# Kernel tuning notes

Hardware: AMD Instinct MI355X
Metric: run time of the kernel (lower is better)

## Reference

```python
import jax, jax.numpy as jnp
import numpy as np

N = 6144      # nodes
NFEAT = 512
NHID = 256
NHEADS = 4
DHEAD = NHID // NHEADS  # 64
NEMBED = 128
NEG_INF = -9e15
LRELU_ALPHA = 0.2


def setup_inputs() -> dict:
    key = jax.random.key(0)
    k = jax.random.split(key, 8)
    x = jax.random.normal(k[0], (N, NFEAT), dtype=jnp.float32)
    adj = (jax.random.uniform(k[1], (N, N)) < 0.01).astype(jnp.int32)
    # per-head GAT params, packed over heads
    W = jax.random.normal(k[2], (NHEADS, NFEAT, DHEAD), dtype=jnp.float32) * 0.05
    a_src = jax.random.normal(k[3], (NHEADS, DHEAD), dtype=jnp.float32) * 0.05
    a_dst = jax.random.normal(k[4], (NHEADS, DHEAD), dtype=jnp.float32) * 0.05
    # output linear (init.normal_ std=0.05 per reset_parameters)
    lin_w = jax.random.normal(k[5], (NEMBED, NHID), dtype=jnp.float32) * 0.05
    lin_b = jnp.zeros((NEMBED,), dtype=jnp.float32)
    return {"x": x, "adj": adj, "W": W, "a_src": a_src, "a_dst": a_dst,
            "lin_w": lin_w, "lin_b": lin_b}


def _gat_forward(x, adj, W, a_src, a_dst, lin_w, lin_b):
    # Wh: [H, N, D]
    Wh = jnp.einsum('nf,hfd->hnd', x, W)
    # attention logits e_ij = leakyrelu(a_src.Wh_i + a_dst.Wh_j): [H, N, N]
    s = jnp.einsum('hnd,hd->hn', Wh, a_src)   # source term per node
    t = jnp.einsum('hnd,hd->hn', Wh, a_dst)   # target term per node
    e = s[:, :, None] + t[:, None, :]
    e = jax.nn.leaky_relu(e, negative_slope=LRELU_ALPHA)
    # mask by adjacency, softmax over neighbors
    e = jnp.where(adj[None, :, :] > 0, e, NEG_INF)
    attn = jax.nn.softmax(e, axis=-1)
    # aggregate and per-head ELU (concat=True GAT layer)
    h = jnp.einsum('hnm,hmd->hnd', attn, Wh)
    h = jax.nn.elu(h)
    # concat heads -> [N, NHID]
    h = jnp.transpose(h, (1, 0, 2)).reshape(N, NHID)
    # dropout is identity in eval mode; linear + ELU
    out = jax.nn.elu(h @ lin_w.T + lin_b)
    return out


def reference(x, adj, W, a_src, a_dst, lin_w, lin_b):
    return _gat_forward(x, adj, W, a_src, a_dst, lin_w, lin_b)
```

## Files before the change

kernel.cpp:

```cpp
#include <hip/hip_runtime.h>
#include <hip/hip_bf16.h>
#include <math.h>

#define N_NODES 6144
#define NFEAT 512
#define NHID 256
#define NHEADS 4
#define DHEAD 64
#define NEMBED 128
#define LRELU_ALPHA 0.2f
#define MAXC 512

__global__ __launch_bounds__(256) void wh_gemm(const float* __restrict__ x,
                                               const float* __restrict__ W,
                                               float* __restrict__ Wh) {
    __shared__ float As[64][16];
    __shared__ float Bs[16][64];
    const int tid = threadIdx.x;
    const int tx = tid & 15;
    const int ty = tid >> 4;
    const int row0 = blockIdx.x * 64;
    const int h = blockIdx.y;
    const float* Bp = W + (size_t)h * NFEAT * DHEAD;

    float acc[4][4] = {};

    for (int k0 = 0; k0 < NFEAT; k0 += 16) {
        {
            const int r = tid >> 2, kq = tid & 3;
            const float4 v = *(const float4*)(x + (size_t)(row0 + r) * NFEAT + k0 + kq * 4);
            *(float4*)&As[r][kq * 4] = v;
        }
        {
            const int kk = tid >> 4, cq = tid & 15;
            const float4 v = *(const float4*)(Bp + (size_t)(k0 + kk) * DHEAD + cq * 4);
            *(float4*)&Bs[kk][cq * 4] = v;
        }
        __syncthreads();
#pragma unroll
        for (int kk = 0; kk < 16; kk++) {
            float a[4], b[4];
#pragma unroll
            for (int i = 0; i < 4; i++) a[i] = As[ty * 4 + i][kk];
#pragma unroll
            for (int j = 0; j < 4; j++) b[j] = Bs[kk][tx * 4 + j];
#pragma unroll
            for (int i = 0; i < 4; i++)
#pragma unroll
                for (int j = 0; j < 4; j++) acc[i][j] += a[i] * b[j];
        }
        __syncthreads();
    }
#pragma unroll
    for (int i = 0; i < 4; i++) {
        const int row = row0 + ty * 4 + i;
        float4 v = make_float4(acc[i][0], acc[i][1], acc[i][2], acc[i][3]);
        *(float4*)(Wh + ((size_t)h * N_NODES + row) * DHEAD + tx * 4) = v;
    }
}

__global__ __launch_bounds__(256) void st_kernel(const float* __restrict__ Wh,
                                                 const float* __restrict__ a_src,
                                                 const float* __restrict__ a_dst,
                                                 float* __restrict__ s_arr,
                                                 float* __restrict__ t_arr) {
    const int n = blockIdx.x;
    const int h = threadIdx.x >> 6;
    const int lane = threadIdx.x & 63;
    const float wh = Wh[((size_t)h * N_NODES + n) * DHEAD + lane];
    float ps = wh * a_src[h * DHEAD + lane];
    float pt = wh * a_dst[h * DHEAD + lane];
#pragma unroll
    for (int off = 32; off > 0; off >>= 1) {
        ps += __shfl_down(ps, off);
        pt += __shfl_down(pt, off);
    }
    if (lane == 0) {
        s_arr[h * N_NODES + n] = ps;
        t_arr[h * N_NODES + n] = pt;
    }
}

__global__ __launch_bounds__(256) void attn_agg(const int* __restrict__ adj,
                                                const float* __restrict__ Wh,
                                                const float* __restrict__ s_arr,
                                                const float* __restrict__ t_arr,
                                                float* __restrict__ hcat) {
    __shared__ unsigned short nbr[N_NODES];
    __shared__ float p_s[NHEADS][MAXC];
    __shared__ int cnt;
    const int i = blockIdx.x;
    const int tid = threadIdx.x;
    if (tid == 0) cnt = 0;
    __syncthreads();

    const int* arow = adj + (size_t)i * N_NODES;
    for (int j0 = tid * 4; j0 < N_NODES; j0 += 1024) {
        const int4 v = *(const int4*)(arow + j0);
        if (v.x) nbr[atomicAdd(&cnt, 1)] = (unsigned short)(j0);
        if (v.y) nbr[atomicAdd(&cnt, 1)] = (unsigned short)(j0 + 1);
        if (v.z) nbr[atomicAdd(&cnt, 1)] = (unsigned short)(j0 + 2);
        if (v.w) nbr[atomicAdd(&cnt, 1)] = (unsigned short)(j0 + 3);
    }
    __syncthreads();
    const int c = cnt;

    const int h = tid >> 6;
    const int lane = tid & 63;
    const float s_h = s_arr[h * N_NODES + i];
    const float* tp = t_arr + (size_t)h * N_NODES;
    const float* whp = Wh + (size_t)h * N_NODES * DHEAD;

    float acc, l;
    if (c > 0 && c <= MAXC) {
        float m = -INFINITY;
        for (int k = lane; k < c; k += 64) {
            float e = s_h + tp[nbr[k]];
            e = e >= 0.0f ? e : LRELU_ALPHA * e;
            p_s[h][k] = e;
            m = fmaxf(m, e);
        }
#pragma unroll
        for (int off = 32; off > 0; off >>= 1) m = fmaxf(m, __shfl_xor(m, off));
        float ls = 0.0f;
        for (int k = lane; k < c; k += 64) {
            const float p = __expf(p_s[h][k] - m);
            p_s[h][k] = p;
            ls += p;
        }
#pragma unroll
        for (int off = 32; off > 0; off >>= 1) ls += __shfl_xor(ls, off);
        l = ls;
        __syncthreads();

        float a0 = 0.0f, a1 = 0.0f, a2 = 0.0f, a3 = 0.0f;
        int k = 0;
        for (; k + 4 <= c; k += 4) {
            const int j0 = nbr[k], j1 = nbr[k + 1], j2 = nbr[k + 2], j3 = nbr[k + 3];
            const float p0 = p_s[h][k], p1 = p_s[h][k + 1],
                        p2 = p_s[h][k + 2], p3 = p_s[h][k + 3];
            a0 += p0 * whp[(size_t)j0 * DHEAD + lane];
            a1 += p1 * whp[(size_t)j1 * DHEAD + lane];
            a2 += p2 * whp[(size_t)j2 * DHEAD + lane];
            a3 += p3 * whp[(size_t)j3 * DHEAD + lane];
        }
        for (; k < c; k++) a0 += p_s[h][k] * whp[(size_t)nbr[k] * DHEAD + lane];
        acc = (a0 + a1) + (a2 + a3);
    } else if (c == 0) {
        acc = 0.0f;
        for (int j = 0; j < N_NODES; j++) acc += whp[(size_t)j * DHEAD + lane];
        l = (float)N_NODES;
    } else {
        float m = -INFINITY, ll = 0.0f;
        acc = 0.0f;
        for (int k = 0; k < c; k++) {
            const int j = nbr[k];
            float e = s_h + tp[j];
            e = e >= 0.0f ? e : LRELU_ALPHA * e;
            const float m_new = fmaxf(m, e);
            const float scale = expf(m - m_new);
            const float p = expf(e - m_new);
            ll = ll * scale + p;
            acc = acc * scale + p * whp[(size_t)j * DHEAD + lane];
            m = m_new;
        }
        l = ll;
    }
    float hv = acc / l;
    hv = hv > 0.0f ? hv : expm1f(hv);
    hcat[(size_t)i * NHID + h * DHEAD + lane] = hv;
}

__global__ __launch_bounds__(256) void out_gemm(const float* __restrict__ hcat,
                                                const float* __restrict__ lin_w,
                                                const float* __restrict__ lin_b,
                                                float* __restrict__ out) {
    __shared__ float As[64][16];
    __shared__ float Bs[16][64];
    const int tid = threadIdx.x;
    const int tx = tid & 15;
    const int ty = tid >> 4;
    const int row0 = blockIdx.x * 64;
    const int c0 = blockIdx.y * 64;

    float acc[4][4] = {};

    for (int k0 = 0; k0 < NHID; k0 += 16) {
        {
            const int r = tid >> 2, kq = tid & 3;
            const float4 v = *(const float4*)(hcat + (size_t)(row0 + r) * NHID + k0 + kq * 4);
            *(float4*)&As[r][kq * 4] = v;
        }
        {
            const int cc = tid & 63, kq = tid >> 6;
            const float4 v = *(const float4*)(lin_w + (size_t)(c0 + cc) * NHID + k0 + kq * 4);
            Bs[kq * 4 + 0][cc] = v.x;
            Bs[kq * 4 + 1][cc] = v.y;
            Bs[kq * 4 + 2][cc] = v.z;
            Bs[kq * 4 + 3][cc] = v.w;
        }
        __syncthreads();
#pragma unroll
        for (int kk = 0; kk < 16; kk++) {
            float a[4], b[4];
#pragma unroll
            for (int i = 0; i < 4; i++) a[i] = As[ty * 4 + i][kk];
#pragma unroll
            for (int j = 0; j < 4; j++) b[j] = Bs[kk][tx * 4 + j];
#pragma unroll
            for (int i = 0; i < 4; i++)
#pragma unroll
                for (int j = 0; j < 4; j++) acc[i][j] += a[i] * b[j];
        }
        __syncthreads();
    }
#pragma unroll
    for (int i = 0; i < 4; i++) {
        const int row = row0 + ty * 4 + i;
        float v[4];
#pragma unroll
        for (int j = 0; j < 4; j++) {
            const int col = c0 + tx * 4 + j;
            float val = acc[i][j] + lin_b[col];
            v[j] = val > 0.0f ? val : expm1f(val);
        }
        *(float4*)(out + (size_t)row * NEMBED + c0 + tx * 4) =
            make_float4(v[0], v[1], v[2], v[3]);
    }
}

extern "C" void kernel_launch(void* const* d_in, const int* in_sizes, int n_in,
                              void* d_out, int out_size, void* d_ws, size_t ws_size,
                              hipStream_t stream) {
    const float* x     = (const float*)d_in[0];
    const int*   adj   = (const int*)d_in[1];
    const float* W     = (const float*)d_in[2];
    const float* a_src = (const float*)d_in[3];
    const float* a_dst = (const float*)d_in[4];
    const float* lin_w = (const float*)d_in[5];
    const float* lin_b = (const float*)d_in[6];
    float* out = (float*)d_out;

    float* Wh   = (float*)d_ws;
    float* s    = Wh + (size_t)NHEADS * N_NODES * DHEAD;
    float* t    = s + (size_t)NHEADS * N_NODES;
    float* hcat = t + (size_t)NHEADS * N_NODES;

    wh_gemm<<<dim3(N_NODES / 64, NHEADS), 256, 0, stream>>>(x, W, Wh);
    st_kernel<<<N_NODES, 256, 0, stream>>>(Wh, a_src, a_dst, s, t);
    attn_agg<<<N_NODES, 256, 0, stream>>>(adj, Wh, s, t, hcat);
    out_gemm<<<dim3(N_NODES / 64, NEMBED / 64), 256, 0, stream>>>(hcat, lin_w, lin_b, out);
}
```

Before: 320.9 us.

## Fuse attention score projection into Wh GEMM and use ballot-based neighbor compaction

Computes the per-node source and target attention scores in the Wh GEMM epilogue through 16-lane xor shuffles, which removes the separate st_kernel launch and its reread of Wh. In attn_agg, neighbor list compaction now uses a wavefront ballot and popcount prefix with one shared atomic per wave, replacing per-element atomics. The aggregation loop is unrolled to 8 independent accumulators, and a redundant barrier is dropped because each wave only reads its own p_s row. MAXC is halved to cut shared memory for occupancy, and the fallback path switches to fast exp; nodes with more than 256 neighbors now take the slower online-softmax path.

```diff
diff --git a/kernel.cpp b/kernel.cpp
--- a/kernel.cpp
+++ b/kernel.cpp
@@ -9,11 +9,15 @@
 #define DHEAD 64
 #define NEMBED 128
 #define LRELU_ALPHA 0.2f
-#define MAXC 512
+#define MAXC 256
 
 __global__ __launch_bounds__(256) void wh_gemm(const float* __restrict__ x,
                                                const float* __restrict__ W,
-                                               float* __restrict__ Wh) {
+                                               const float* __restrict__ a_src,
+                                               const float* __restrict__ a_dst,
+                                               float* __restrict__ Wh,
+                                               float* __restrict__ s_arr,
+                                               float* __restrict__ t_arr) {
     __shared__ float As[64][16];
     __shared__ float Bs[16][64];
     const int tid = threadIdx.x;
@@ -57,27 +61,28 @@
         float4 v = make_float4(acc[i][0], acc[i][1], acc[i][2], acc[i][3]);
         *(float4*)(Wh + ((size_t)h * N_NODES + row) * DHEAD + tx * 4) = v;
     }
-}
-
-__global__ __launch_bounds__(256) void st_kernel(const float* __restrict__ Wh,
-                                                 const float* __restrict__ a_src,
-                                                 const float* __restrict__ a_dst,
-                                                 float* __restrict__ s_arr,
-                                                 float* __restrict__ t_arr) {
-    const int n = blockIdx.x;
-    const int h = threadIdx.x >> 6;
-    const int lane = threadIdx.x & 63;
-    const float wh = Wh[((size_t)h * N_NODES + n) * DHEAD + lane];
-    float ps = wh * a_src[h * DHEAD + lane];
-    float pt = wh * a_dst[h * DHEAD + lane];
-#pragma unroll
-    for (int off = 32; off > 0; off >>= 1) {
-        ps += __shfl_down(ps, off);
-        pt += __shfl_down(pt, off);
-    }
-    if (lane == 0) {
-        s_arr[h * N_NODES + n] = ps;
-        t_arr[h * N_NODES + n] = pt;
+    float a4s[4], a4d[4];
+#pragma unroll
+    for (int j = 0; j < 4; j++) {
+        a4s[j] = a_src[h * DHEAD + tx * 4 + j];
+        a4d[j] = a_dst[h * DHEAD + tx * 4 + j];
+    }
+#pragma unroll
+    for (int i = 0; i < 4; i++) {
+        float ps = acc[i][0] * a4s[0] + acc[i][1] * a4s[1] +
+                   acc[i][2] * a4s[2] + acc[i][3] * a4s[3];
+        float pt = acc[i][0] * a4d[0] + acc[i][1] * a4d[1] +
+                   acc[i][2] * a4d[2] + acc[i][3] * a4d[3];
+#pragma unroll
+        for (int off = 1; off < 16; off <<= 1) {
+            ps += __shfl_xor(ps, off);
+            pt += __shfl_xor(pt, off);
+        }
+        if (tx == 0) {
+            const int row = row0 + ty * 4 + i;
+            s_arr[h * N_NODES + row] = ps;
+            t_arr[h * N_NODES + row] = pt;
+        }
     }
 }
 
@@ -91,22 +96,39 @@
     __shared__ int cnt;
     const int i = blockIdx.x;
     const int tid = threadIdx.x;
+    const int wid = tid >> 6;
+    const int lane = tid & 63;
     if (tid == 0) cnt = 0;
     __syncthreads();
 
     const int* arow = adj + (size_t)i * N_NODES;
-    for (int j0 = tid * 4; j0 < N_NODES; j0 += 1024) {
+    const unsigned long long lower = (1ull << lane) - 1ull;
+#pragma unroll
+    for (int it = 0; it < 6; ++it) {
+        const int j0 = it * 1024 + wid * 256 + lane * 4;
         const int4 v = *(const int4*)(arow + j0);
-        if (v.x) nbr[atomicAdd(&cnt, 1)] = (unsigned short)(j0);
-        if (v.y) nbr[atomicAdd(&cnt, 1)] = (unsigned short)(j0 + 1);
-        if (v.z) nbr[atomicAdd(&cnt, 1)] = (unsigned short)(j0 + 2);
-        if (v.w) nbr[atomicAdd(&cnt, 1)] = (unsigned short)(j0 + 3);
+        const unsigned long long b0 = __ballot(v.x != 0);
+        const unsigned long long b1 = __ballot(v.y != 0);
+        const unsigned long long b2 = __ballot(v.z != 0);
+        const unsigned long long b3 = __ballot(v.w != 0);
+        const int n0 = __popcll(b0), n1 = __popcll(b1);
+        const int n2 = __popcll(b2), n3 = __popcll(b3);
+        const int tot = n0 + n1 + n2 + n3;
+        int base = 0;
+        if (lane == 0 && tot) base = atomicAdd(&cnt, tot);
+        base = __shfl(base, 0);
+        if (v.x) nbr[base + __popcll(b0 & lower)] = (unsigned short)j0;
+        base += n0;
+        if (v.y) nbr[base + __popcll(b1 & lower)] = (unsigned short)(j0 + 1);
+        base += n1;
+        if (v.z) nbr[base + __popcll(b2 & lower)] = (unsigned short)(j0 + 2);
+        base += n2;
+        if (v.w) nbr[base + __popcll(b3 & lower)] = (unsigned short)(j0 + 3);
     }
     __syncthreads();
     const int c = cnt;
 
-    const int h = tid >> 6;
-    const int lane = tid & 63;
+    const int h = wid;
     const float s_h = s_arr[h * N_NODES + i];
     const float* tp = t_arr + (size_t)h * N_NODES;
     const float* whp = Wh + (size_t)h * N_NODES * DHEAD;
@@ -131,21 +153,28 @@
 #pragma unroll
         for (int off = 32; off > 0; off >>= 1) ls += __shfl_xor(ls, off);
         l = ls;
-        __syncthreads();
-
-        float a0 = 0.0f, a1 = 0.0f, a2 = 0.0f, a3 = 0.0f;
+
+        float a0 = 0.f, a1 = 0.f, a2 = 0.f, a3 = 0.f;
+        float a4 = 0.f, a5 = 0.f, a6 = 0.f, a7 = 0.f;
         int k = 0;
-        for (; k + 4 <= c; k += 4) {
-            const int j0 = nbr[k], j1 = nbr[k + 1], j2 = nbr[k + 2], j3 = nbr[k + 3];
-            const float p0 = p_s[h][k], p1 = p_s[h][k + 1],
-                        p2 = p_s[h][k + 2], p3 = p_s[h][k + 3];
+        for (; k + 8 <= c; k += 8) {
+            const int j0 = nbr[k],     j1 = nbr[k + 1], j2 = nbr[k + 2], j3 = nbr[k + 3];
+            const int j4 = nbr[k + 4], j5 = nbr[k + 5], j6 = nbr[k + 6], j7 = nbr[k + 7];
+            const float p0 = p_s[h][k],     p1 = p_s[h][k + 1];
+            const float p2 = p_s[h][k + 2], p3 = p_s[h][k + 3];
+            const float p4 = p_s[h][k + 4], p5 = p_s[h][k + 5];
+            const float p6 = p_s[h][k + 6], p7 = p_s[h][k + 7];
             a0 += p0 * whp[(size_t)j0 * DHEAD + lane];
             a1 += p1 * whp[(size_t)j1 * DHEAD + lane];
             a2 += p2 * whp[(size_t)j2 * DHEAD + lane];
             a3 += p3 * whp[(size_t)j3 * DHEAD + lane];
+            a4 += p4 * whp[(size_t)j4 * DHEAD + lane];
+            a5 += p5 * whp[(size_t)j5 * DHEAD + lane];
+            a6 += p6 * whp[(size_t)j6 * DHEAD + lane];
+            a7 += p7 * whp[(size_t)j7 * DHEAD + lane];
         }
         for (; k < c; k++) a0 += p_s[h][k] * whp[(size_t)nbr[k] * DHEAD + lane];
-        acc = (a0 + a1) + (a2 + a3);
+        acc = ((a0 + a1) + (a2 + a3)) + ((a4 + a5) + (a6 + a7));
     } else if (c == 0) {
         acc = 0.0f;
         for (int j = 0; j < N_NODES; j++) acc += whp[(size_t)j * DHEAD + lane];
@@ -158,8 +187,8 @@
             float e = s_h + tp[j];
             e = e >= 0.0f ? e : LRELU_ALPHA * e;
             const float m_new = fmaxf(m, e);
-            const float scale = expf(m - m_new);
-            const float p = expf(e - m_new);
+            const float scale = __expf(m - m_new);
+            const float p = __expf(e - m_new);
             ll = ll * scale + p;
             acc = acc * scale + p * whp[(size_t)j * DHEAD + lane];
             m = m_new;
@@ -246,8 +275,7 @@
     float* t    = s + (size_t)NHEADS * N_NODES;
     float* hcat = t + (size_t)NHEADS * N_NODES;
 
-    wh_gemm<<<dim3(N_NODES / 64, NHEADS), 256, 0, stream>>>(x, W, Wh);
-    st_kernel<<<N_NODES, 256, 0, stream>>>(Wh, a_src, a_dst, s, t);
+    wh_gemm<<<dim3(N_NODES / 64, NHEADS), 256, 0, stream>>>(x, W, a_src, a_dst, Wh, s, t);
     attn_agg<<<N_NODES, 256, 0, stream>>>(adj, Wh, s, t, hcat);
     out_gemm<<<dim3(N_NODES / 64, NEMBED / 64), 256, 0, stream>>>(hcat, lin_w, lin_b, out);
 }
```

Result: faster. 308.0 us (-4.0%).
